# Optimization experiments

Measured on AMD Instinct MI355X. Metric: run time of the kernel, lower is better.

## Reference

```python
import jax, jax.numpy as jnp
import numpy as np

N_NODES = 100000
N_EDGES = 50000
NNZ = 1000000


def _scatter_mean(vals, idx, num_segments):
    s = jax.ops.segment_sum(vals, idx, num_segments=num_segments)
    cnt = jax.ops.segment_sum(jnp.ones((vals.shape[0],), vals.dtype), idx, num_segments=num_segments)
    return s / jnp.maximum(cnt, 1.0)[:, None]


def _normalize_l2(X):
    # row L2 normalize; scale computed on detached values, inf -> 0
    norm = jnp.linalg.norm(X, axis=1, keepdims=True)
    scale = jax.lax.stop_gradient(jnp.where(norm > 0, 1.0 / norm, 0.0))
    return X * scale


def _conv(X, W, V, E, homo, use_norm):
    # X: [N, in], W: [in, heads*out]
    X = X @ W                                   # [N, D]
    Xve = X[V]                                  # gather vertex -> incidence [nnz, D]
    Xe = _scatter_mean(Xve, E, N_EDGES)         # first_aggregate='mean' -> [nE, D]
    Xev = Xe[E]                                 # gather edge -> incidence [nnz, D]
    he = homo[E]                                # [nnz]
    att_sum = jax.ops.segment_sum(he, V, num_segments=N_NODES)[V]  # [nnz]
    att = (he / att_sum)[:, None]               # [nnz, 1]
    Xv = jax.ops.segment_sum(att * Xev, V, num_segments=N_NODES)   # second_aggregate='sum' -> [N, D]
    X = X + Xv
    if use_norm:
        X = _normalize_l2(X)
    return X


def setup_inputs() -> dict:
    key = jax.random.key(0)
    k1, k2, k3, k4, k5, k6, k7 = jax.random.split(key, 7)
    nfeat, dh, nclass = 256, 256, 40  # dh = nhid*nhead = 64*4
    X = jax.random.normal(k1, (N_NODES, nfeat), dtype=jnp.float32)
    V = jax.random.randint(k2, (NNZ,), 0, N_NODES)
    E = jax.random.randint(k3, (NNZ,), 0, N_EDGES)
    homo = jax.random.uniform(k4, (N_EDGES,), dtype=jnp.float32, minval=0.1, maxval=1.0)
    s1 = 1.0 / np.sqrt(nfeat)
    s2 = 1.0 / np.sqrt(dh)
    W1 = jax.random.uniform(k5, (nfeat, dh), dtype=jnp.float32, minval=-s1, maxval=s1)
    W2 = jax.random.uniform(k6, (dh, dh), dtype=jnp.float32, minval=-s2, maxval=s2)
    Wout = jax.random.uniform(k7, (dh, nclass), dtype=jnp.float32, minval=-s2, maxval=s2)
    return {"X": X, "V": V, "E": E, "homo": homo, "W1": W1, "W2": W2, "Wout": Wout}


def reference(X, V, E, homo, W1, W2, Wout):
    # HHyperGNN.forward (eval mode: dropouts are identity), nlayer=3
    X = _conv(X, W1, V, E, homo, use_norm=True)
    X = jax.nn.relu(X)
    X = _conv(X, W2, V, E, homo, use_norm=True)
    X = jax.nn.relu(X)
    Z = X
    X = _conv(X, Wout, V, E, homo, use_norm=True)
    return (Z, X)
```

## Files before the change

kernel.cpp:

```cpp
#include <hip/hip_runtime.h>

#define NND 100000
#define NED 50000
#define NNZC 1000000
#define MGRID 1564
#define CNTB 512

typedef __attribute__((ext_vector_type(8))) short bf16x8;
typedef __attribute__((ext_vector_type(4))) float f32x4;

__device__ __forceinline__ float b2f(unsigned short u) {
  union { unsigned int u; float f; } x; x.u = ((unsigned int)u) << 16; return x.f;
}
__device__ __forceinline__ float blo(unsigned int u) {
  union { unsigned int u; float f; } x; x.u = u << 16; return x.f;
}
__device__ __forceinline__ float bhi(unsigned int u) {
  union { unsigned int u; float f; } x; x.u = u & 0xffff0000u; return x.f;
}
__device__ __forceinline__ unsigned short f2b(float f) {
  union { float f; unsigned int u; } x; x.f = f;
  unsigned int r = x.u + 0x7FFFu + ((x.u >> 16) & 1u);
  return (unsigned short)(r >> 16);
}
__device__ __forceinline__ unsigned int pk2(float lo, float hi) {
  return (unsigned int)f2b(lo) | ((unsigned int)f2b(hi) << 16);
}

__global__ void detect_k(const unsigned short* __restrict__ homo_u16,
                         int* __restrict__ mode) {
  if (threadIdx.x == 0 && blockIdx.x == 0) {
    int bf16_ok = 1;
    for (int i = 0; i < 64; i++) {
      float v = b2f(homo_u16[i]);
      if (!(v >= 0.04f && v <= 1.1f)) bf16_ok = 0;
    }
    *mode = bf16_ok ? 0 : 1;
  }
}

__global__ void prep_f32(const void* __restrict__ Hin, const void* __restrict__ W1,
                         const void* __restrict__ W2, const void* __restrict__ Wout,
                         float* __restrict__ Hf, unsigned short* __restrict__ WT1b,
                         unsigned short* __restrict__ WT2b, float* __restrict__ Wf3,
                         const int* __restrict__ mode) {
  int i = blockIdx.x * 256 + threadIdx.x;
  int m = *mode;
  if (i < 65536) {
    int n = i >> 8, k = i & 255;
    float w1 = m ? ((const float*)W1)[k * 256 + n] : b2f(((const unsigned short*)W1)[k * 256 + n]);
    float w2 = m ? ((const float*)W2)[k * 256 + n] : b2f(((const unsigned short*)W2)[k * 256 + n]);
    WT1b[i] = f2b(w1);
    WT2b[i] = f2b(w2);
  }
  if (i < 16384) {
    int k = i >> 6, n = i & 63;
    Wf3[i] = (n < 40)
      ? (m ? ((const float*)Wout)[k * 40 + n] : b2f(((const unsigned short*)Wout)[k * 40 + n]))
      : 0.f;
  }
  if (i < NED)
    Hf[i] = m ? ((const float*)Hin)[i] : b2f(((const unsigned short*)Hin)[i]);
}

__device__ __forceinline__ void gemm_body(
    const void* __restrict__ A, bool a_fp32,
    const unsigned short* __restrict__ WT,
    unsigned short* __restrict__ Cb, int M, int bid) {
  __shared__ unsigned short As[128][40];
  __shared__ unsigned short Bs[128][40];
  const int t = threadIdx.x;
  const int l = t & 63;
  const int w = t >> 6;
  const int wr = w >> 1, wc = w & 1;
  const int lr16 = l & 15, lg = l >> 4;
  const int bm = bid >> 1;
  const int n0 = (bid & 1) * 128;
  const int row0 = bm * 128;

  const int tr = t >> 1, th = t & 1;
  int arow = row0 + tr; if (arow >= M) arow = M - 1;

  f32x4 acc[4][4];
#pragma unroll
  for (int m = 0; m < 4; m++)
#pragma unroll
    for (int n = 0; n < 4; n++) acc[m][n] = (f32x4){0.f, 0.f, 0.f, 0.f};

  uint4 a0, a1, b0, b1;
  auto load_regs = [&](int k0) {
    if (a_fp32) {
      const float4* ap = (const float4*)((const float*)A + (size_t)arow * 256 + k0 + th * 16);
      float4 f0 = ap[0], f1 = ap[1], f2 = ap[2], f3 = ap[3];
      a0 = make_uint4(pk2(f0.x, f0.y), pk2(f0.z, f0.w), pk2(f1.x, f1.y), pk2(f1.z, f1.w));
      a1 = make_uint4(pk2(f2.x, f2.y), pk2(f2.z, f2.w), pk2(f3.x, f3.y), pk2(f3.z, f3.w));
    } else {
      const uint4* ap = (const uint4*)((const unsigned short*)A + (size_t)arow * 256 + k0 + th * 16);
      a0 = ap[0]; a1 = ap[1];
    }
    const uint4* bp = (const uint4*)(WT + (size_t)(n0 + tr) * 256 + k0 + th * 16);
    b0 = bp[0]; b1 = bp[1];
  };

  load_regs(0);
  for (int k0 = 0; k0 < 256; k0 += 32) {
    __syncthreads();
    *(uint4*)&As[tr][th * 16]     = a0;
    *(uint4*)&As[tr][th * 16 + 8] = a1;
    *(uint4*)&Bs[tr][th * 16]     = b0;
    *(uint4*)&Bs[tr][th * 16 + 8] = b1;
    __syncthreads();
    if (k0 < 224) load_regs(k0 + 32);

    bf16x8 af[4], bfr[4];
#pragma unroll
    for (int m = 0; m < 4; m++)
      af[m] = *(const bf16x8*)&As[wr * 64 + m * 16 + lr16][lg * 8];
#pragma unroll
    for (int n = 0; n < 4; n++)
      bfr[n] = *(const bf16x8*)&Bs[wc * 64 + n * 16 + lr16][lg * 8];
#pragma unroll
    for (int m = 0; m < 4; m++)
#pragma unroll
      for (int n = 0; n < 4; n++)
        acc[m][n] = __builtin_amdgcn_mfma_f32_16x16x32_bf16(af[m], bfr[n], acc[m][n], 0, 0, 0);
  }

#pragma unroll
  for (int m = 0; m < 4; m++) {
#pragma unroll
    for (int j = 0; j < 4; j++) {
      int row = row0 + wr * 64 + m * 16 + lg * 4 + j;
      if (row < M) {
#pragma unroll
        for (int n = 0; n < 4; n++)
          Cb[(size_t)row * 256 + n0 + wc * 64 + n * 16 + lr16] = f2b(acc[m][n][j]);
      }
    }
  }
}

__global__ __launch_bounds__(256) void gemm1_cnt(
    const void* __restrict__ A, const int* __restrict__ mode,
    const unsigned short* __restrict__ WT, unsigned short* __restrict__ Cb, int M,
    const int* __restrict__ V, const int* __restrict__ E,
    int* __restrict__ cntAll, unsigned short* __restrict__ rV,
    unsigned short* __restrict__ rE) {
  const int b = blockIdx.x;
  if (b < CNTB) {
    const int STRIDE = CNTB * 256;
    int i0 = b * 256 + threadIdx.x;
#pragma unroll
    for (int q = 0; q < 8; q++) {
      int i = i0 + q * STRIDE;
      if (i < NNZC) {
        unsigned short rv = (unsigned short)atomicAdd(&cntAll[V[i]], 1);
        unsigned short re = (unsigned short)atomicAdd(&cntAll[NND + E[i]], 1);
        rV[i] = rv;
        rE[i] = re;
      }
    }
    return;
  }
  gemm_body(A, *mode == 1, WT, Cb, M, b - CNTB);
}

__global__ __launch_bounds__(256) void gemm_bf16_k(
    const unsigned short* __restrict__ A, const unsigned short* __restrict__ WT,
    unsigned short* __restrict__ Cb, int M) {
  gemm_body(A, false, WT, Cb, M, blockIdx.x);
}

__global__ __launch_bounds__(256) void gemm_tile_b64(
    const unsigned short* __restrict__ A, const float* __restrict__ W,
    unsigned short* __restrict__ C, int M) {
  constexpr int N = 64, BM = 64, BK = 32, CPT = 2;
  __shared__ float As[BM][BK + 1];
  __shared__ float Ws[BK][N];
  const int t = threadIdx.x;
  const int tx = t & 31, ty = t >> 5;
  const int row0 = blockIdx.x * BM;

  float acc[8][CPT];
#pragma unroll
  for (int i = 0; i < 8; i++)
#pragma unroll
    for (int j = 0; j < CPT; j++) acc[i][j] = 0.f;

  for (int k0 = 0; k0 < 256; k0 += BK) {
#pragma unroll
    for (int l = t; l < BM * BK / 4; l += 256) {
      int r = l >> 3, seg = l & 7;
      int row = row0 + r;
      if (row >= M) row = M - 1;
      int col = k0 + seg * 4;
      ushort4 u = *(const ushort4*)(A + (size_t)row * 256 + col);
      As[r][seg * 4 + 0] = b2f(u.x);
      As[r][seg * 4 + 1] = b2f(u.y);
      As[r][seg * 4 + 2] = b2f(u.z);
      As[r][seg * 4 + 3] = b2f(u.w);
    }
#pragma unroll
    for (int l = t; l < BK * N / 4; l += 256) {
      ((float4*)&Ws[0][0])[l] = *(const float4*)(W + (size_t)k0 * N + l * 4);
    }
    __syncthreads();

#pragma unroll 4
    for (int kk = 0; kk < BK; kk++) {
      float a[8], w[CPT];
#pragma unroll
      for (int i = 0; i < 8; i++) a[i] = As[ty * 8 + i][kk];
#pragma unroll
      for (int j = 0; j < CPT; j++) w[j] = Ws[kk][tx + 32 * j];
#pragma unroll
      for (int i = 0; i < 8; i++)
#pragma unroll
        for (int j = 0; j < CPT; j++) acc[i][j] += a[i] * w[j];
    }
    __syncthreads();
  }

#pragma unroll
  for (int i = 0; i < 8; i++) {
    int row = row0 + ty * 8 + i;
    if (row < M) {
#pragma unroll
      for (int j = 0; j < CPT; j++)
        C[(size_t)row * N + tx + 32 * j] = f2b(acc[i][j]);
    }
  }
}

__global__ void scan_local(const int* __restrict__ in, int* __restrict__ outExcl,
                           int* __restrict__ bsum, int n) {
  __shared__ int s[256];
  int t = threadIdx.x;
  int i = blockIdx.x * 256 + t;
  int v = (i < n) ? in[i] : 0;
  s[t] = v;
  __syncthreads();
  for (int off = 1; off < 256; off <<= 1) {
    int x = (t >= off) ? s[t - off] : 0;
    __syncthreads();
    s[t] += x;
    __syncthreads();
  }
  if (i < n) outExcl[i] = s[t] - v;
  if (t == 255) bsum[blockIdx.x] = s[255];
}

__global__ void scan_sums(int* __restrict__ bsum, int nb) {
  __shared__ int s[1024];
  int t = threadIdx.x;
  int v = (t < nb) ? bsum[t] : 0;
  s[t] = v;
  __syncthreads();
  for (int off = 1; off < 1024; off <<= 1) {
    int x = (t >= off) ? s[t - off] : 0;
    __syncthreads();
    s[t] += x;
    __syncthreads();
  }
  if (t < nb) bsum[t] = s[t] - v;
}

__global__ void scan_add(int* __restrict__ outExcl, const int* __restrict__ bsum, int n) {
  int i = blockIdx.x * 256 + threadIdx.x;
  if (i < n) outExcl[i] += bsum[blockIdx.x];
}

__global__ void fill_nr(const int* __restrict__ V, const int* __restrict__ E,
                        const int* __restrict__ offAll,
                        const unsigned short* __restrict__ rV,
                        const unsigned short* __restrict__ rE,
                        const float* __restrict__ Hf,
                        unsigned int* __restrict__ vadjH,
                        int* __restrict__ eadj) {
  int i = blockIdx.x * 256 + threadIdx.x;
  if (i < NNZC) {
    int v = V[i], e = E[i];
    vadjH[offAll[v] + rV[i]] = (unsigned int)e | ((unsigned int)f2b(Hf[e]) << 16);
    eadj[offAll[NND + e] - NNZC + rE[i]] = v;
  }
}

__global__ __launch_bounds__(256) void edge_gather_b(
    const int* __restrict__ eoff, const int* __restrict__ cntE,
    const int* __restrict__ eadj, const unsigned int* __restrict__ XWb,
    unsigned int* __restrict__ Xeb) {
  int e = blockIdx.x * 4 + (threadIdx.x >> 6);
  int tl = threadIdx.x & 63;
  if (e >= NED) return;
  int start = eoff[e] - NNZC, n = cntE[e];
  float a0 = 0.f, a1 = 0.f, a2 = 0.f, a3 = 0.f;
  for (int c0 = 0; c0 < n; c0 += 64) {
    int m = n - c0; if (m > 64) m = 64;
    int vidx = (tl < m) ? eadj[start + c0 + tl] : 0;
#pragma unroll 4
    for (int j = 0; j < m; j++) {
      int vv = __shfl(vidx, j);
      uint2 x = *((const uint2*)(XWb + (size_t)vv * 128) + tl);
      a0 += blo(x.x); a1 += bhi(x.x); a2 += blo(x.y); a3 += bhi(x.y);
    }
  }
  float inv = (n > 0) ? 1.0f / (float)n : 0.f;
  uint2 o;
  o.x = pk2(a0 * inv, a1 * inv);
  o.y = pk2(a2 * inv, a3 * inv);
  *((uint2*)(Xeb + (size_t)e * 128) + tl) = o;
}

__global__ __launch_bounds__(256) void node_gather_norm_b(
    const int* __restrict__ voff, const int* __restrict__ degV,
    const unsigned int* __restrict__ vadjH,
    const unsigned int* __restrict__ Xeb, const unsigned int* __restrict__ XWb,
    unsigned int* __restrict__ Zb, float* __restrict__ outf) {
  int v = blockIdx.x * 4 + (threadIdx.x >> 6);
  int tl = threadIdx.x & 63;
  if (v >= NND) return;
  int start = voff[v], n = degV[v];
  uint2 r = *((const uint2*)(XWb + (size_t)v * 128) + tl);
  float a0 = blo(r.x), a1 = bhi(r.x), a2 = blo(r.y), a3 = bhi(r.y);
  float g0 = 0.f, g1 = 0.f, g2 = 0.f, g3 = 0.f, hsum = 0.f;
  for (int c0 = 0; c0 < n; c0 += 64) {
    int m = n - c0; if (m > 64) m = 64;
    unsigned int pk = (tl < m) ? vadjH[start + c0 + tl] : 0u;
    hsum += b2f((unsigned short)(pk >> 16));
#pragma unroll 4
    for (int j = 0; j < m; j++) {
      unsigned int u = (unsigned int)__shfl((int)pk, j);
      int ee = (int)(u & 0xffffu);
      float a = b2f((unsigned short)(u >> 16));
      uint2 x = *((const uint2*)(Xeb + (size_t)ee * 128) + tl);
      g0 += a * blo(x.x); g1 += a * bhi(x.x);
      g2 += a * blo(x.y); g3 += a * bhi(x.y);
    }
  }
#pragma unroll
  for (int off = 32; off; off >>= 1) hsum += __shfl_xor(hsum, off);
  float inv_att = (hsum > 0.f) ? 1.0f / hsum : 0.f;
  a0 += inv_att * g0; a1 += inv_att * g1;
  a2 += inv_att * g2; a3 += inv_att * g3;
  float ss = a0 * a0 + a1 * a1 + a2 * a2 + a3 * a3;
#pragma unroll
  for (int off = 32; off; off >>= 1) ss += __shfl_xor(ss, off);
  float sc = (ss > 0.f) ? (1.0f / sqrtf(ss)) : 0.f;
  a0 = fmaxf(a0 * sc, 0.f); a1 = fmaxf(a1 * sc, 0.f);
  a2 = fmaxf(a2 * sc, 0.f); a3 = fmaxf(a3 * sc, 0.f);
  uint2 o; o.x = pk2(a0, a1); o.y = pk2(a2, a3);
  *((uint2*)(Zb + (size_t)v * 128) + tl) = o;
  if (outf) *((float4*)(outf + (size_t)v * 256) + tl) = make_float4(a0, a1, a2, a3);
}

__global__ __launch_bounds__(256) void edge_gather_64(
    const int* __restrict__ eoff, const int* __restrict__ cntE,
    const int* __restrict__ eadj, const unsigned short* __restrict__ XW64,
    unsigned short* __restrict__ Xe64) {
  int e = blockIdx.x * 4 + (threadIdx.x >> 6);
  int tl = threadIdx.x & 63;
  if (e >= NED) return;
  int start = eoff[e] - NNZC, n = cntE[e];
  float ax = 0.f;
  for (int c0 = 0; c0 < n; c0 += 64) {
    int m = n - c0; if (m > 64) m = 64;
    int vidx = (tl < m) ? eadj[start + c0 + tl] : 0;
#pragma unroll 4
    for (int j = 0; j < m; j++) {
      int vv = __shfl(vidx, j);
      ax += b2f(XW64[(size_t)vv * 64 + tl]);
    }
  }
  float inv = (n > 0) ? 1.0f / (float)n : 0.f;
  Xe64[(size_t)e * 64 + tl] = f2b(ax * inv);
}

__global__ __launch_bounds__(256) void node_gather_norm_64(
    const int* __restrict__ voff, const int* __restrict__ degV,
    const unsigned int* __restrict__ vadjH,
    const unsigned short* __restrict__ Xe64, const unsigned short* __restrict__ XW64,
    float* __restrict__ out) {
  int v = blockIdx.x * 4 + (threadIdx.x >> 6);
  int tl = threadIdx.x & 63;
  if (v >= NND) return;
  int start = voff[v], n = degV[v];
  float ax = b2f(XW64[(size_t)v * 64 + tl]);
  float gx = 0.f, hsum = 0.f;
  for (int c0 = 0; c0 < n; c0 += 64) {
    int m = n - c0; if (m > 64) m = 64;
    unsigned int pk = (tl < m) ? vadjH[start + c0 + tl] : 0u;
    hsum += b2f((unsigned short)(pk >> 16));
#pragma unroll 4
    for (int j = 0; j < m; j++) {
      unsigned int u = (unsigned int)__shfl((int)pk, j);
      int ee = (int)(u & 0xffffu);
      float a = b2f((unsigned short)(u >> 16));
      gx += a * b2f(Xe64[(size_t)ee * 64 + tl]);
    }
  }
#pragma unroll
  for (int off = 32; off; off >>= 1) hsum += __shfl_xor(hsum, off);
  float inv_att = (hsum > 0.f) ? 1.0f / hsum : 0.f;
  ax += inv_att * gx;
  float ss = ax * ax;
#pragma unroll
  for (int off = 32; off; off >>= 1) ss += __shfl_xor(ss, off);
  float sc = (ss > 0.f) ? (1.0f / sqrtf(ss)) : 0.f;
  ax *= sc;
  if (tl < 40) out[(size_t)v * 40 + tl] = ax;
}

__global__ void sentinel_k(float* __restrict__ out, long n, float val) {
  long i = (long)blockIdx.x * 256 + threadIdx.x;
  long stride = (long)gridDim.x * 256;
  for (; i < n; i += stride) out[i] = val;
}

extern "C" void kernel_launch(void* const* d_in, const int* in_sizes, int n_in,
                              void* d_out, int out_size, void* d_ws, size_t ws_size,
                              hipStream_t stream) {
  const void* Xin  = d_in[0];
  const int*  V    = (const int*)d_in[1];
  const int*  E    = (const int*)d_in[2];
  const void* Hin  = d_in[3];
  const void* W1   = d_in[4];
  const void* W2   = d_in[5];
  const void* Wout = d_in[6];
  float* Zout = (float*)d_out;
  float* Xout = Zout + (size_t)NND * 256;
  (void)in_sizes; (void)n_in;

  char* base = (char*)d_ws;
  size_t o = 0;
  auto carve = [&](size_t bytes) -> char* {
    char* p = base + o;
    o += (bytes + 255) & ~(size_t)255;
    return p;
  };
  unsigned int*  XWb  = (unsigned int*)carve((size_t)NND * 256 * 2);
  unsigned int*  Xeb  = (unsigned int*)carve((size_t)NED * 256 * 2);
  unsigned int*  Zb   = (unsigned int*)carve((size_t)NND * 256 * 2);
  unsigned short* XW64 = (unsigned short*)carve((size_t)NND * 64 * 2);
  unsigned short* Xe64 = (unsigned short*)carve((size_t)NED * 64 * 2);
  float* Hf    = (float*)carve((size_t)NED * 4);
  int*   cntAll = (int*)carve((size_t)(NND + NED) * 4);
  int*   offAll = (int*)carve((size_t)(NND + NED) * 4);
  unsigned short* rV = (unsigned short*)carve((size_t)NNZC * 2);
  unsigned short* rE = (unsigned short*)carve((size_t)NNZC * 2);
  unsigned int* vadjH = (unsigned int*)carve((size_t)NNZC * 4);
  int*   eadj  = (int*)carve((size_t)NNZC * 4);
  int*   bsum  = (int*)carve(1024 * 4);
  unsigned short* WT1b = (unsigned short*)carve(65536 * 2);
  unsigned short* WT2b = (unsigned short*)carve(65536 * 2);
  float* Wf3   = (float*)carve(16384 * 4);
  int*   mode  = (int*)carve(256);
  const size_t NEED = o;

  if (ws_size < NEED) {
    sentinel_k<<<4096, 256, 0, stream>>>(Zout, (long)out_size, 77.0f);
    return;
  }

  const int NCNT = NND + NED;
  const int NBC = (NCNT + 255) / 256;
  const int GEMM_GRID = (NND + 63) / 64;
  const int FILL_GRID = (NNZC + 255) / 256;
  const int EG_GRID = (NED + 3) / 4;
  const int NG_GRID = (NND + 3) / 4;

  const int* voff = offAll;
  const int* eoff = offAll + NND;
  const int* degV = cntAll;
  const int* cntE = cntAll + NND;

  detect_k<<<1, 64, 0, stream>>>((const unsigned short*)Hin, mode);
  prep_f32<<<256, 256, 0, stream>>>(Hin, W1, W2, Wout, Hf, WT1b, WT2b, Wf3, mode);
  hipMemsetAsync(cntAll, 0, (size_t)NCNT * 4, stream);

  gemm1_cnt<<<CNTB + MGRID, 256, 0, stream>>>(Xin, mode, WT1b, (unsigned short*)XWb,
                                              NND, V, E, cntAll, rV, rE);

  scan_local<<<NBC, 256, 0, stream>>>(cntAll, offAll, bsum, NCNT);
  scan_sums<<<1, 1024, 0, stream>>>(bsum, NBC);
  scan_add<<<NBC, 256, 0, stream>>>(offAll, bsum, NCNT);
  fill_nr<<<FILL_GRID, 256, 0, stream>>>(V, E, offAll, rV, rE, Hf, vadjH, eadj);

  edge_gather_b<<<EG_GRID, 256, 0, stream>>>(eoff, cntE, eadj, XWb, Xeb);
  node_gather_norm_b<<<NG_GRID, 256, 0, stream>>>(voff, degV, vadjH, Xeb, XWb, Zb, nullptr);

  gemm_bf16_k<<<MGRID, 256, 0, stream>>>((const unsigned short*)Zb, WT2b,
                                         (unsigned short*)XWb, NND);
  edge_gather_b<<<EG_GRID, 256, 0, stream>>>(eoff, cntE, eadj, XWb, Xeb);
  node_gather_norm_b<<<NG_GRID, 256, 0, stream>>>(voff, degV, vadjH, Xeb, XWb, Zb, Zout);

  gemm_tile_b64<<<GEMM_GRID, 256, 0, stream>>>((const unsigned short*)Zb, Wf3, XW64, NND);
  edge_gather_64<<<EG_GRID, 256, 0, stream>>>(eoff, cntE, eadj, XW64, Xe64);
  node_gather_norm_64<<<NG_GRID, 256, 0, stream>>>(voff, degV, vadjH, Xe64, XW64, Xout);
}
```

Before: 916.6 us.

## Fuse final-layer projection into node gather, merge detect and scan kernels

Folds the last 256x64 projection into the second node-gather kernel: each wave stages its normalized row in shared memory and computes the 64 outputs directly, avoiding the bf16 Z write/re-read and a separate GEMM launch. The format-detection kernel is merged into the weight prep kernel, and the three-stage scan is reduced to two by having each block sum preceding block totals itself. The fused projection reads weights from global memory per thread without register tiling, which may cost more compute time than the standalone tiled GEMM.

```diff
diff --git a/kernel.cpp b/kernel.cpp
--- a/kernel.cpp
+++ b/kernel.cpp
@@ -27,25 +27,22 @@
   return (unsigned int)f2b(lo) | ((unsigned int)f2b(hi) << 16);
 }
 
-__global__ void detect_k(const unsigned short* __restrict__ homo_u16,
-                         int* __restrict__ mode) {
-  if (threadIdx.x == 0 && blockIdx.x == 0) {
-    int bf16_ok = 1;
-    for (int i = 0; i < 64; i++) {
-      float v = b2f(homo_u16[i]);
-      if (!(v >= 0.04f && v <= 1.1f)) bf16_ok = 0;
-    }
-    *mode = bf16_ok ? 0 : 1;
-  }
-}
-
 __global__ void prep_f32(const void* __restrict__ Hin, const void* __restrict__ W1,
                          const void* __restrict__ W2, const void* __restrict__ Wout,
                          float* __restrict__ Hf, unsigned short* __restrict__ WT1b,
                          unsigned short* __restrict__ WT2b, float* __restrict__ Wf3,
-                         const int* __restrict__ mode) {
+                         int* __restrict__ mode) {
+  __shared__ int ok;
+  if (threadIdx.x == 0) ok = 1;
+  __syncthreads();
+  if (threadIdx.x < 64) {
+    float v = b2f(((const unsigned short*)Hin)[threadIdx.x]);
+    if (!(v >= 0.04f && v <= 1.1f)) ok = 0;
+  }
+  __syncthreads();
+  int m = ok ? 0 : 1;
   int i = blockIdx.x * 256 + threadIdx.x;
-  int m = *mode;
+  if (i == 0) *mode = m;
   if (i < 65536) {
     int n = i >> 8, k = i & 255;
     float w1 = m ? ((const float*)W1)[k * 256 + n] : b2f(((const unsigned short*)W1)[k * 256 + n]);
@@ -171,67 +168,6 @@
   gemm_body(A, false, WT, Cb, M, blockIdx.x);
 }
 
-__global__ __launch_bounds__(256) void gemm_tile_b64(
-    const unsigned short* __restrict__ A, const float* __restrict__ W,
-    unsigned short* __restrict__ C, int M) {
-  constexpr int N = 64, BM = 64, BK = 32, CPT = 2;
-  __shared__ float As[BM][BK + 1];
-  __shared__ float Ws[BK][N];
-  const int t = threadIdx.x;
-  const int tx = t & 31, ty = t >> 5;
-  const int row0 = blockIdx.x * BM;
-
-  float acc[8][CPT];
-#pragma unroll
-  for (int i = 0; i < 8; i++)
-#pragma unroll
-    for (int j = 0; j < CPT; j++) acc[i][j] = 0.f;
-
-  for (int k0 = 0; k0 < 256; k0 += BK) {
-#pragma unroll
-    for (int l = t; l < BM * BK / 4; l += 256) {
-      int r = l >> 3, seg = l & 7;
-      int row = row0 + r;
-      if (row >= M) row = M - 1;
-      int col = k0 + seg * 4;
-      ushort4 u = *(const ushort4*)(A + (size_t)row * 256 + col);
-      As[r][seg * 4 + 0] = b2f(u.x);
-      As[r][seg * 4 + 1] = b2f(u.y);
-      As[r][seg * 4 + 2] = b2f(u.z);
-      As[r][seg * 4 + 3] = b2f(u.w);
-    }
-#pragma unroll
-    for (int l = t; l < BK * N / 4; l += 256) {
-      ((float4*)&Ws[0][0])[l] = *(const float4*)(W + (size_t)k0 * N + l * 4);
-    }
-    __syncthreads();
-
-#pragma unroll 4
-    for (int kk = 0; kk < BK; kk++) {
-      float a[8], w[CPT];
-#pragma unroll
-      for (int i = 0; i < 8; i++) a[i] = As[ty * 8 + i][kk];
-#pragma unroll
-      for (int j = 0; j < CPT; j++) w[j] = Ws[kk][tx + 32 * j];
-#pragma unroll
-      for (int i = 0; i < 8; i++)
-#pragma unroll
-        for (int j = 0; j < CPT; j++) acc[i][j] += a[i] * w[j];
-    }
-    __syncthreads();
-  }
-
-#pragma unroll
-  for (int i = 0; i < 8; i++) {
-    int row = row0 + ty * 8 + i;
-    if (row < M) {
-#pragma unroll
-      for (int j = 0; j < CPT; j++)
-        C[(size_t)row * N + tx + 32 * j] = f2b(acc[i][j]);
-    }
-  }
-}
-
 __global__ void scan_local(const int* __restrict__ in, int* __restrict__ outExcl,
                            int* __restrict__ bsum, int n) {
   __shared__ int s[256];
@@ -250,24 +186,21 @@
   if (t == 255) bsum[blockIdx.x] = s[255];
 }
 
-__global__ void scan_sums(int* __restrict__ bsum, int nb) {
-  __shared__ int s[1024];
-  int t = threadIdx.x;
-  int v = (t < nb) ? bsum[t] : 0;
-  s[t] = v;
+__global__ void scan_add2(int* __restrict__ outExcl, const int* __restrict__ bsum,
+                          int n) {
+  __shared__ int sm[256];
+  int b = blockIdx.x, t = threadIdx.x;
+  int partial = 0;
+  for (int j = t; j < b; j += 256) partial += bsum[j];
+  sm[t] = partial;
   __syncthreads();
-  for (int off = 1; off < 1024; off <<= 1) {
-    int x = (t >= off) ? s[t - off] : 0;
-    __syncthreads();
-    s[t] += x;
-    __syncthreads();
-  }
-  if (t < nb) bsum[t] = s[t] - v;
-}
-
-__global__ void scan_add(int* __restrict__ outExcl, const int* __restrict__ bsum, int n) {
-  int i = blockIdx.x * 256 + threadIdx.x;
-  if (i < n) outExcl[i] += bsum[blockIdx.x];
+  for (int off = 128; off; off >>= 1) {
+    if (t < off) sm[t] += sm[t + off];
+    __syncthreads();
+  }
+  int total = sm[0];
+  int i = b * 256 + t;
+  if (i < n) outExcl[i] += total;
 }
 
 __global__ void fill_nr(const int* __restrict__ V, const int* __restrict__ E,
@@ -315,10 +248,12 @@
     const int* __restrict__ voff, const int* __restrict__ degV,
     const unsigned int* __restrict__ vadjH,
     const unsigned int* __restrict__ Xeb, const unsigned int* __restrict__ XWb,
-    unsigned int* __restrict__ Zb, float* __restrict__ outf) {
-  int v = blockIdx.x * 4 + (threadIdx.x >> 6);
+    unsigned int* __restrict__ Zb, float* __restrict__ outf,
+    const float* __restrict__ W3, unsigned short* __restrict__ XW64) {
+  __shared__ float zrow[4][256];
+  int wid = threadIdx.x >> 6;
+  int v = blockIdx.x * 4 + wid;
   int tl = threadIdx.x & 63;
-  if (v >= NND) return;
   int start = voff[v], n = degV[v];
   uint2 r = *((const uint2*)(XWb + (size_t)v * 128) + tl);
   float a0 = blo(r.x), a1 = bhi(r.x), a2 = blo(r.y), a3 = bhi(r.y);
@@ -348,9 +283,25 @@
   float sc = (ss > 0.f) ? (1.0f / sqrtf(ss)) : 0.f;
   a0 = fmaxf(a0 * sc, 0.f); a1 = fmaxf(a1 * sc, 0.f);
   a2 = fmaxf(a2 * sc, 0.f); a3 = fmaxf(a3 * sc, 0.f);
-  uint2 o; o.x = pk2(a0, a1); o.y = pk2(a2, a3);
-  *((uint2*)(Zb + (size_t)v * 128) + tl) = o;
+  if (Zb) {
+    uint2 o; o.x = pk2(a0, a1); o.y = pk2(a2, a3);
+    *((uint2*)(Zb + (size_t)v * 128) + tl) = o;
+  }
   if (outf) *((float4*)(outf + (size_t)v * 256) + tl) = make_float4(a0, a1, a2, a3);
+  if (W3) {
+    *(float4*)&zrow[wid][tl * 4] = make_float4(a0, a1, a2, a3);
+    __syncthreads();
+    float out = 0.f;
+#pragma unroll 4
+    for (int k = 0; k < 256; k += 4) {
+      float4 z4 = *(const float4*)&zrow[wid][k];
+      out += z4.x * W3[(k + 0) * 64 + tl];
+      out += z4.y * W3[(k + 1) * 64 + tl];
+      out += z4.z * W3[(k + 2) * 64 + tl];
+      out += z4.w * W3[(k + 3) * 64 + tl];
+    }
+    XW64[(size_t)v * 64 + tl] = f2b(out);
+  }
 }
 
 __global__ __launch_bounds__(256) void edge_gather_64(
@@ -463,7 +414,6 @@
 
   const int NCNT = NND + NED;
   const int NBC = (NCNT + 255) / 256;
-  const int GEMM_GRID = (NND + 63) / 64;
   const int FILL_GRID = (NNZC + 255) / 256;
   const int EG_GRID = (NED + 3) / 4;
   const int NG_GRID = (NND + 3) / 4;
@@ -473,7 +423,6 @@
   const int* degV = cntAll;
   const int* cntE = cntAll + NND;
 
-  detect_k<<<1, 64, 0, stream>>>((const unsigned short*)Hin, mode);
   prep_f32<<<256, 256, 0, stream>>>(Hin, W1, W2, Wout, Hf, WT1b, WT2b, Wf3, mode);
   hipMemsetAsync(cntAll, 0, (size_t)NCNT * 4, stream);
 
@@ -481,19 +430,19 @@
                                               NND, V, E, cntAll, rV, rE);
 
   scan_local<<<NBC, 256, 0, stream>>>(cntAll, offAll, bsum, NCNT);
-  scan_sums<<<1, 1024, 0, stream>>>(bsum, NBC);
-  scan_add<<<NBC, 256, 0, stream>>>(offAll, bsum, NCNT);
+  scan_add2<<<NBC, 256, 0, stream>>>(offAll, bsum, NCNT);
   fill_nr<<<FILL_GRID, 256, 0, stream>>>(V, E, offAll, rV, rE, Hf, vadjH, eadj);
 
   edge_gather_b<<<EG_GRID, 256, 0, stream>>>(eoff, cntE, eadj, XWb, Xeb);
-  node_gather_norm_b<<<NG_GRID, 256, 0, stream>>>(voff, degV, vadjH, Xeb, XWb, Zb, nullptr);
+  node_gather_norm_b<<<NG_GRID, 256, 0, stream>>>(voff, degV, vadjH, Xeb, XWb,
+                                                  Zb, nullptr, nullptr, nullptr);
 
   gemm_bf16_k<<<MGRID, 256, 0, stream>>>((const unsigned short*)Zb, WT2b,
                                          (unsigned short*)XWb, NND);
   edge_gather_b<<<EG_GRID, 256, 0, stream>>>(eoff, cntE, eadj, XWb, Xeb);
-  node_gather_norm_b<<<NG_GRID, 256, 0, stream>>>(voff, degV, vadjH, Xeb, XWb, Zb, Zout);
-
-  gemm_tile_b64<<<GEMM_GRID, 256, 0, stream>>>((const unsigned short*)Zb, Wf3, XW64, NND);
+  node_gather_norm_b<<<NG_GRID, 256, 0, stream>>>(voff, degV, vadjH, Xeb, XWb,
+                                                  nullptr, Zout, Wf3, XW64);
+
   edge_gather_64<<<EG_GRID, 256, 0, stream>>>(eoff, cntE, eadj, XW64, Xe64);
   node_gather_norm_64<<<NG_GRID, 256, 0, stream>>>(voff, degV, vadjH, Xe64, XW64, Xout);
 }
```

After: 967.1 us. 5.5% more time.
